# Kernel tuning notes

Measured on AMD Instinct MI355X. Metric: run time of the kernel, lower is better.

## Reference

```python
import jax, jax.numpy as jnp
import numpy as np

TRUST_W, SIM_W, STALE_W = 0.4, 0.4, 0.2
EPS = 1e-8  # torch cosine_similarity norm clamp


def setup_inputs() -> dict:
    key = jax.random.key(0)
    ks = jax.random.split(key, 6)
    B, D, E, C = 8192, 1024, 32, 256
    x = jax.random.normal(ks[0], (B, D), dtype=jnp.float32)
    expert_features = jax.random.normal(ks[1], (E, D), dtype=jnp.float32)
    trust = jax.random.uniform(ks[2], (E,), dtype=jnp.float32)
    staleness = jax.random.uniform(ks[3], (E,), dtype=jnp.float32)
    W = jax.random.normal(ks[4], (E, C, D), dtype=jnp.float32) * 0.02
    b = jax.random.normal(ks[5], (E, C), dtype=jnp.float32) * 0.02
    return {"x": x, "expert_features": expert_features, "trust": trust,
            "staleness": staleness, "W": W, "b": b, "k": 4}


def reference(x, expert_features, trust, staleness, W, b, k):
    # --- scoring: trust + cosine similarity + staleness, per (token, expert) ---
    xn = x / jnp.maximum(jnp.linalg.norm(x, axis=-1, keepdims=True), EPS)
    efn = expert_features / jnp.maximum(
        jnp.linalg.norm(expert_features, axis=-1, keepdims=True), EPS)
    cos = xn @ efn.T                              # [B, E]
    sim = (cos + 1.0) * 0.5
    stale_score = jnp.maximum(0.0, 1.0 - staleness)  # [E]
    scores = TRUST_W * trust + SIM_W * sim + STALE_W * stale_score  # [B, E]

    # --- top-k expert selection per token ---
    _, idx = jax.lax.top_k(scores, k)             # [B, k] int32

    # --- grouped expert heads: dense all-expert GEMM, then gather top-k ---
    all_out = jnp.einsum('bd,ecd->bec', x, W) + b  # [B, E, C]
    sel = jnp.take_along_axis(all_out, idx[:, :, None], axis=1)  # [B, k, C]
    return sel.mean(axis=1)                        # [B, C]
```

## Files before the change

### kernel.cpp

```cpp
#include <hip/hip_runtime.h>
#include <math.h>

#define KMAX 8
#define CSTRIDE 64

typedef short s16x8 __attribute__((ext_vector_type(8)));
typedef float f32x4 __attribute__((ext_vector_type(4)));

__device__ inline ushort f2bf(float f) {
    union { float f; unsigned u; } v; v.f = f;
    unsigned r = v.u + 0x7fffu + ((v.u >> 16) & 1u);
    return (ushort)(r >> 16);
}
__device__ inline float bf2f(ushort b) {
    union { unsigned u; float f; } v; v.u = ((unsigned)b) << 16; return v.f;
}

__device__ inline void gload_lds16(const void* g, void* l) {
    __builtin_amdgcn_global_load_lds(
        (const __attribute__((address_space(1))) unsigned int*)g,
        (__attribute__((address_space(3))) unsigned int*)l, 16, 0, 0);
}

__global__ void k_efnorm(const float* __restrict__ ef, int D,
                         double* __restrict__ efn, int* __restrict__ counts) {
    int e = blockIdx.x;
    int lane = threadIdx.x;
    if (lane == 0) counts[e * CSTRIDE] = 0;
    double s = 0.0;
    for (int i = lane; i < D; i += 64) {
        double v = (double)ef[(size_t)e * D + i];
        s = fma(v, v, s);
    }
    #pragma unroll
    for (int off = 32; off > 0; off >>= 1) s += __shfl_xor(s, off);
    if (lane == 0) efn[e] = sqrt(s);
}

__global__ __launch_bounds__(256) void k_prep_w(
    const float* __restrict__ W, const int* __restrict__ counts,
    int perExpF4, ushort* __restrict__ wbf, int* __restrict__ offs) {
    int e = blockIdx.y;
    if (blockIdx.x == 0 && e == 0 && threadIdx.x == 0) {
        int s = 0;
        for (int e2 = 0; e2 < 32; ++e2) { offs[e2] = s; s += counts[e2 * CSTRIDE]; }
    }
    if (counts[e * CSTRIDE] == 0) return;
    size_t base = (size_t)e * perExpF4;
    #pragma unroll
    for (int j = 0; j < 4; ++j) {
        int idx = (blockIdx.x * 4 + j) * 256 + threadIdx.x;
        if (idx < perExpF4) {
            float4 v = *(const float4*)&W[(base + idx) * 4];
            ushort4 u;
            u.x = f2bf(v.x); u.y = f2bf(v.y); u.z = f2bf(v.z); u.w = f2bf(v.w);
            *(ushort4*)&wbf[(base + idx) * 4] = u;
        }
    }
}

__global__ __launch_bounds__(256) void k_scores3a(
    const float* __restrict__ x, const float* __restrict__ ef,
    int D, int B, ushort* __restrict__ xbf,
    double* __restrict__ pacc, double* __restrict__ paxx)
{
    __shared__ float xs[16 * 64];
    __shared__ float efs[32 * 64];

    int tid = threadIdx.x;
    int tp = tid >> 4, eg = tid & 15;
    int g = blockIdx.x >> 1, h = blockIdx.x & 1;
    int tb = g * 16;
    int kbase = h * (D >> 1);
    int nch = D >> 7;

    int rx = tid >> 4, qx = tid & 15;
    int re0 = tid >> 4, re1 = 16 + (tid >> 4);
    int qe = tid & 15;

    float4 vx  = *(const float4*)&x[(size_t)(tb + rx) * D + kbase + qx * 4];
    float4 ve0 = *(const float4*)&ef[(size_t)re0 * D + kbase + qe * 4];
    float4 ve1 = *(const float4*)&ef[(size_t)re1 * D + kbase + qe * 4];

    double acc0 = 0.0, acc1 = 0.0, axx = 0.0;

    for (int ch = 0; ch < nch; ++ch) {
        int k0 = kbase + ch * 64;
        *(float4*)&xs[rx * 64 + ((qx ^ rx) << 2)] = vx;
        {
            ushort4 u;
            u.x = f2bf(vx.x); u.y = f2bf(vx.y); u.z = f2bf(vx.z); u.w = f2bf(vx.w);
            *(ushort4*)&xbf[(size_t)(tb + rx) * D + k0 + qx * 4] = u;
        }
        *(float4*)&efs[re0 * 64 + ((qe ^ (re0 & 15)) << 2)] = ve0;
        *(float4*)&efs[re1 * 64 + ((qe ^ (re1 & 15)) << 2)] = ve1;
        __syncthreads();

        if (ch + 1 < nch) {
            int k1 = kbase + (ch + 1) * 64;
            vx  = *(const float4*)&x[(size_t)(tb + rx) * D + k1 + qx * 4];
            ve0 = *(const float4*)&ef[(size_t)re0 * D + k1 + qe * 4];
            ve1 = *(const float4*)&ef[(size_t)re1 * D + k1 + qe * 4];
        }

        float a0 = 0.f, a1 = 0.f, ax = 0.f;
        #pragma unroll
        for (int q = 0; q < 16; ++q) {
            float4 xv = *(const float4*)&xs[tp * 64 + ((q ^ tp) << 2)];
            float4 e0 = *(const float4*)&efs[eg * 64 + ((q ^ eg) << 2)];
            float4 e1 = *(const float4*)&efs[(eg + 16) * 64 + ((q ^ eg) << 2)];
            a0 = fmaf(xv.x, e0.x, a0); a0 = fmaf(xv.y, e0.y, a0);
            a0 = fmaf(xv.z, e0.z, a0); a0 = fmaf(xv.w, e0.w, a0);
            a1 = fmaf(xv.x, e1.x, a1); a1 = fmaf(xv.y, e1.y, a1);
            a1 = fmaf(xv.z, e1.z, a1); a1 = fmaf(xv.w, e1.w, a1);
            ax = fmaf(xv.x, xv.x, ax); ax = fmaf(xv.y, xv.y, ax);
            ax = fmaf(xv.z, xv.z, ax); ax = fmaf(xv.w, xv.w, ax);
        }
        __syncthreads();
        acc0 += (double)a0; acc1 += (double)a1; axx += (double)ax;
    }

    int tt = tb + tp;
    pacc[(size_t)(h * 32 + eg) * B + tt] = acc0;
    pacc[(size_t)(h * 32 + eg + 16) * B + tt] = acc1;
    if (eg == 0) paxx[(size_t)h * B + tt] = axx;
}

__global__ __launch_bounds__(256) void k_scores3b(
    const float* __restrict__ trust, const float* __restrict__ stale,
    const double* __restrict__ efn, const double* __restrict__ pacc,
    const double* __restrict__ paxx, const int* __restrict__ kp,
    int B, int* __restrict__ counts, int* __restrict__ lists,
    int* __restrict__ sel)
{
    __shared__ double sc[128 * 33];
    __shared__ int bcnt[32];
    __shared__ int bbase[32];
    __shared__ unsigned char selb[128 * KMAX];
    __shared__ unsigned char lposb[128 * KMAX];

    int tid = threadIdx.x;
    int tk = tid & 127, eh = tid >> 7;
    int t = blockIdx.x * 128 + tk;

    if (tid < 32) bcnt[tid] = 0;

    double axx = paxx[t] + paxx[(size_t)B + t];
    double xn = fmax(sqrt(axx), 1e-8);
    #pragma unroll
    for (int j = 0; j < 16; ++j) {
        int e = eh * 16 + j;
        double dot = pacc[(size_t)e * B + t] + pacc[(size_t)(32 + e) * B + t];
        double en = fmax(efn[e], 1e-8);
        sc[tk * 33 + e] = 0.4 * (double)trust[e]
            + 0.2 * (dot / (xn * en) + 1.0)
            + 0.2 * fmax(0.0, 1.0 - (double)stale[e]);
    }
    __syncthreads();

    int kk = kp[0]; kk = kk < 1 ? 1 : (kk > KMAX ? KMAX : kk);

    if (tid < 128) {
        unsigned mask = 0;
        for (int p = 0; p < kk; ++p) {
            double bv = -1e300; int be = 0;
            #pragma unroll
            for (int e = 0; e < 32; ++e) {
                double v = sc[tid * 33 + e];
                if (!((mask >> e) & 1u) && v > bv) { bv = v; be = e; }
            }
            mask |= 1u << be;
            selb[tid * KMAX + p] = (unsigned char)be;
            lposb[tid * KMAX + p] = (unsigned char)atomicAdd(&bcnt[be], 1);
        }
    }
    __syncthreads();
    if (tid < 32) {
        int c = bcnt[tid];
        bbase[tid] = c ? atomicAdd(&counts[tid * CSTRIDE], c) : 0;
    }
    __syncthreads();
    if (tid < 128) {
        int tt = blockIdx.x * 128 + tid;
        for (int p = 0; p < kk; ++p) {
            int e = selb[tid * KMAX + p];
            int pos = bbase[e] + lposb[tid * KMAX + p];
            lists[(size_t)e * B + pos] = tt;
            sel[(size_t)tt * KMAX + p] = (e << 24) | pos;
        }
    }
}

__global__ __launch_bounds__(512) void k_moe3(
    const ushort* __restrict__ xbf, const ushort* __restrict__ wbf,
    const float* __restrict__ bias, const int* __restrict__ lists,
    const int* __restrict__ counts, const int* __restrict__ offs,
    const int* __restrict__ kp, int B, int C, int D,
    int usePart, ushort* __restrict__ part, float* __restrict__ out)
{
    int e = blockIdx.z;
    int cnt = counts[e * CSTRIDE];
    int row0 = blockIdx.x * 128;
    if (row0 >= cnt) return;
    int col0 = blockIdx.y * 128;
    int nt = min(128, cnt - row0);

    __shared__ ushort xs[128 * 64];
    __shared__ ushort wsh[128 * 64];
    __shared__ int toks[128];

    int tid = threadIdx.x;
    if (tid < 128) toks[tid] = (tid < nt) ? lists[(size_t)e * B + row0 + tid] : 0;
    __syncthreads();

    int lane = tid & 63, wid = tid >> 6;
    int wr = wid >> 1, wc = wid & 1;
    int l15 = lane & 15, l16 = lane >> 4;

    f32x4 acc[2][4];
    #pragma unroll
    for (int m = 0; m < 2; ++m)
        #pragma unroll
        for (int n = 0; n < 4; ++n) acc[m][n] = (f32x4){0.f, 0.f, 0.f, 0.f};

    int nch = D / 64;
    for (int ch = 0; ch < nch; ++ch) {
        int k0 = ch * 64;
        #pragma unroll
        for (int t = 0; t < 2; ++t) {
            int id = t * 512 + tid;
            int r = id >> 3, seg = id & 7;
            int ssw = (seg ^ (r & 7)) << 3;
            gload_lds16(&xbf[(size_t)toks[r] * D + k0 + ssw],
                        (char*)xs + (size_t)(t * 512 + wid * 64) * 16);
        }
        #pragma unroll
        for (int t = 0; t < 2; ++t) {
            int id = t * 512 + tid;
            int r = id >> 3, seg = id & 7;
            int ssw = (seg ^ (r & 7)) << 3;
            gload_lds16(&wbf[((size_t)e * C + col0 + r) * D + k0 + ssw],
                        (char*)wsh + (size_t)(t * 512 + wid * 64) * 16);
        }
        __syncthreads();
        #pragma unroll
        for (int ks = 0; ks < 2; ++ks) {
            s16x8 a[2], bfr[4];
            int sbase = ks * 4 + l16;
            #pragma unroll
            for (int m = 0; m < 2; ++m) {
                int r = wr * 32 + m * 16 + l15;
                a[m] = *(const s16x8*)&xs[r * 64 + ((sbase ^ (l15 & 7)) << 3)];
            }
            #pragma unroll
            for (int n = 0; n < 4; ++n) {
                int r = wc * 64 + n * 16 + l15;
                bfr[n] = *(const s16x8*)&wsh[r * 64 + ((sbase ^ (l15 & 7)) << 3)];
            }
            #pragma unroll
            for (int m = 0; m < 2; ++m)
                #pragma unroll
                for (int n = 0; n < 4; ++n)
                    acc[m][n] = __builtin_amdgcn_mfma_f32_16x16x32_bf16(
                        a[m], bfr[n], acc[m][n], 0, 0, 0);
        }
        __syncthreads();
    }

    int kk = kp[0]; kk = kk < 1 ? 1 : (kk > KMAX ? KMAX : kk);
    if (usePart) {
        int slotBase = offs[e] + row0;
        #pragma unroll
        for (int m = 0; m < 2; ++m) {
            int rbase = wr * 32 + m * 16 + l16 * 4;
            #pragma unroll
            for (int n = 0; n < 4; ++n) {
                int col = col0 + wc * 64 + n * 16 + l15;
                float bv = bias[(size_t)e * C + col];
                #pragma unroll
                for (int r = 0; r < 4; ++r) {
                    int rl = rbase + r;
                    if (rl < nt)
                        part[(size_t)(slotBase + rl) * C + col] =
                            f2bf(acc[m][n][r] + bv);
                }
            }
        }
    } else {
        float invk = 1.0f / (float)kk;
        #pragma unroll
        for (int m = 0; m < 2; ++m) {
            int rbase = wr * 32 + m * 16 + l16 * 4;
            #pragma unroll
            for (int n = 0; n < 4; ++n) {
                int col = col0 + wc * 64 + n * 16 + l15;
                float bv = bias[(size_t)e * C + col];
                #pragma unroll
                for (int r = 0; r < 4; ++r) {
                    int rl = rbase + r;
                    if (rl < nt)
                        atomicAdd(&out[(size_t)toks[rl] * C + col],
                                  invk * (acc[m][n][r] + bv));
                }
            }
        }
    }
}

__global__ __launch_bounds__(256) void k_combine(
    const ushort* __restrict__ part, const int* __restrict__ sel,
    const int* __restrict__ offs, const int* __restrict__ kp,
    int C, float* __restrict__ out)
{
    int kk = kp[0]; kk = kk < 1 ? 1 : (kk > KMAX ? KMAX : kk);
    float invk = 1.0f / (float)kk;
    int sub = threadIdx.x >> 6, lane = threadIdx.x & 63;
    int t = blockIdx.x * 4 + sub;
    for (int c = lane * 4; c < C; c += 256) {
        float s0 = 0.f, s1 = 0.f, s2 = 0.f, s3 = 0.f;
        for (int p = 0; p < kk; ++p) {
            int sv = sel[(size_t)t * KMAX + p];
            int slot = offs[sv >> 24] + (sv & 0xFFFFFF);
            ushort4 u = *(const ushort4*)&part[(size_t)slot * C + c];
            s0 += bf2f(u.x); s1 += bf2f(u.y); s2 += bf2f(u.z); s3 += bf2f(u.w);
        }
        float4 o = make_float4(invk * s0, invk * s1, invk * s2, invk * s3);
        *(float4*)&out[(size_t)t * C + c] = o;
    }
}

__global__ __launch_bounds__(256) void k_scores_legacy(
    const float* __restrict__ x, const float* __restrict__ ef,
    const float* __restrict__ trust, const float* __restrict__ stale,
    const double* __restrict__ efn, const int* __restrict__ kp,
    int D, int B, int* __restrict__ counts, int* __restrict__ lists)
{
    __shared__ float xs[32][72];
    __shared__ float efs[32][72];
    __shared__ double sc[32][33];

    int tid = threadIdx.x;
    int tl = tid >> 3, eg = tid & 7;
    int tb = blockIdx.x * 32;

    double acc[4] = {0, 0, 0, 0};
    double axx = 0.0;
    int nch = D / 64;

    for (int ch = 0; ch < nch; ++ch) {
        #pragma unroll
        for (int t = 0; t < 2; ++t) {
            int id = t * 256 + tid;
            int r = id >> 4, q = id & 15;
            float4 v = *(const float4*)&x[(size_t)(tb + r) * D + ch * 64 + q * 4];
            *(float4*)&xs[r][q * 4] = v;
            float4 w = *(const float4*)&ef[(size_t)r * D + ch * 64 + q * 4];
            *(float4*)&efs[r][q * 4] = w;
        }
        __syncthreads();
        #pragma unroll 4
        for (int q = 0; q < 16; ++q) {
            float4 xv = *(const float4*)&xs[tl][q * 4];
            double x0 = xv.x, x1 = xv.y, x2 = xv.z, x3 = xv.w;
            axx = fma(x0, x0, fma(x1, x1, fma(x2, x2, fma(x3, x3, axx))));
            #pragma unroll
            for (int j = 0; j < 4; ++j) {
                float4 ev = *(const float4*)&efs[eg + 8 * j][q * 4];
                acc[j] = fma(x0, (double)ev.x, acc[j]);
                acc[j] = fma(x1, (double)ev.y, acc[j]);
                acc[j] = fma(x2, (double)ev.z, acc[j]);
                acc[j] = fma(x3, (double)ev.w, acc[j]);
            }
        }
        __syncthreads();
    }

    double xn = fmax(sqrt(axx), 1e-8);
    #pragma unroll
    for (int j = 0; j < 4; ++j) {
        int e = eg + 8 * j;
        double en = fmax(efn[e], 1e-8);
        double cosv = acc[j] / (xn * en);
        sc[tl][e] = 0.4 * (double)trust[e] + 0.2 * (cosv + 1.0)
                  + 0.2 * fmax(0.0, 1.0 - (double)stale[e]);
    }
    __syncthreads();

    if (tid < 32) {
        int kk = kp[0]; kk = kk < 1 ? 1 : (kk > KMAX ? KMAX : kk);
        unsigned mask = 0;
        int t = tb + tid;
        for (int p = 0; p < kk; ++p) {
            double bv = -1e300; int be = 0;
            #pragma unroll
            for (int e = 0; e < 32; ++e) {
                double v = sc[tid][e];
                if (!((mask >> e) & 1u) && v > bv) { bv = v; be = e; }
            }
            mask |= 1u << be;
            int pos = atomicAdd(&counts[be * CSTRIDE], 1);
            lists[(size_t)be * B + pos] = t;
        }
    }
}

__global__ __launch_bounds__(512) void k_moe_f32(
    const float* __restrict__ x, const float* __restrict__ W,
    const float* __restrict__ bias, const int* __restrict__ lists,
    const int* __restrict__ counts, const int* __restrict__ kp,
    int B, int C, int D, float* __restrict__ out)
{
    int e = blockIdx.z;
    int cnt = counts[e * CSTRIDE];
    int row0 = blockIdx.x * 128;
    if (row0 >= cnt) return;
    int col0 = blockIdx.y * 256;
    int nt = min(128, cnt - row0);

    __shared__ ushort xs[128 * 72];
    __shared__ ushort wsh[256 * 72];
    __shared__ int toks[128];

    int tid = threadIdx.x;
    if (tid < 128) toks[tid] = (tid < nt) ? lists[(size_t)e * B + row0 + tid] : 0;
    __syncthreads();

    int lane = tid & 63, wid = tid >> 6;
    int wr = wid >> 2, wc = wid & 3;
    int l15 = lane & 15, l16 = lane >> 4;

    f32x4 acc[4][4];
    #pragma unroll
    for (int m = 0; m < 4; ++m)
        #pragma unroll
        for (int n = 0; n < 4; ++n) acc[m][n] = (f32x4){0.f, 0.f, 0.f, 0.f};

    int nch = D / 64;
    for (int ch = 0; ch < nch; ++ch) {
        int k0 = ch * 64;
        #pragma unroll
        for (int t = 0; t < 4; ++t) {
            int id = t * 512 + tid;
            int r = id >> 4, q = id & 15;
            float4 v = (r < nt)
                ? *(const float4*)&x[(size_t)toks[r] * D + k0 + q * 4]
                : make_float4(0.f, 0.f, 0.f, 0.f);
            ushort4 u;
            u.x = f2bf(v.x); u.y = f2bf(v.y); u.z = f2bf(v.z); u.w = f2bf(v.w);
            *(ushort4*)&xs[r * 72 + q * 4] = u;
        }
        #pragma unroll
        for (int t = 0; t < 8; ++t) {
            int id = t * 512 + tid;
            int r = id >> 4, q = id & 15;
            float4 v = *(const float4*)&W[((size_t)e * C + col0 + r) * D + k0 + q * 4];
            ushort4 u;
            u.x = f2bf(v.x); u.y = f2bf(v.y); u.z = f2bf(v.z); u.w = f2bf(v.w);
            *(ushort4*)&wsh[r * 72 + q * 4] = u;
        }
        __syncthreads();
        #pragma unroll
        for (int ks = 0; ks < 2; ++ks) {
            s16x8 a[4], bfr[4];
            #pragma unroll
            for (int m = 0; m < 4; ++m)
                a[m] = *(const s16x8*)&xs[(wr * 64 + m * 16 + l15) * 72 + ks * 32 + l16 * 8];
            #pragma unroll
            for (int n = 0; n < 4; ++n)
                bfr[n] = *(const s16x8*)&wsh[(wc * 64 + n * 16 + l15) * 72 + ks * 32 + l16 * 8];
            #pragma unroll
            for (int m = 0; m < 4; ++m)
                #pragma unroll
                for (int n = 0; n < 4; ++n)
                    acc[m][n] = __builtin_amdgcn_mfma_f32_16x16x32_bf16(
                        a[m], bfr[n], acc[m][n], 0, 0, 0);
        }
        __syncthreads();
    }

    int kk = kp[0]; kk = kk < 1 ? 1 : (kk > KMAX ? KMAX : kk);
    float invk = 1.0f / (float)kk;
    #pragma unroll
    for (int m = 0; m < 4; ++m) {
        int rbase = wr * 64 + m * 16 + l16 * 4;
        #pragma unroll
        for (int n = 0; n < 4; ++n) {
            int col = col0 + wc * 64 + n * 16 + l15;
            float bv = bias[(size_t)e * C + col];
            #pragma unroll
            for (int r = 0; r < 4; ++r) {
                int rl = rbase + r;
                if (rl < nt)
                    atomicAdd(&out[(size_t)toks[rl] * C + col],
                              invk * (acc[m][n][r] + bv));
            }
        }
    }
}

extern "C" void kernel_launch(void* const* d_in, const int* in_sizes, int n_in,
                              void* d_out, int out_size, void* d_ws, size_t ws_size,
                              hipStream_t stream) {
    const float* x     = (const float*)d_in[0];
    const float* ef    = (const float*)d_in[1];
    const float* trust = (const float*)d_in[2];
    const float* stale = (const float*)d_in[3];
    const float* W     = (const float*)d_in[4];
    const float* b     = (const float*)d_in[5];
    const int*   kp    = (const int*)d_in[6];

    int E = in_sizes[2];
    int D = in_sizes[1] / E;
    int B = in_sizes[0] / D;
    int C = in_sizes[5] / E;
    float* out = (float*)d_out;

    char* ws = (char*)d_ws;
    double* efn   = (double*)ws;
    int*    counts= (int*)(ws + 256);
    size_t off_offs = 256 + 32 * CSTRIDE * 4;
    int*    offs  = (int*)(ws + off_offs);
    size_t off_sel = off_offs + 256;
    int*    sel   = (int*)(ws + off_sel);
    size_t off_lists = off_sel + (size_t)B * KMAX * 4;
    int*    lists = (int*)(ws + off_lists);
    size_t off_pacc = off_lists + (size_t)E * B * 4;
    off_pacc = (off_pacc + 255) & ~(size_t)255;
    double* pacc  = (double*)(ws + off_pacc);
    size_t off_paxx = off_pacc + (size_t)64 * B * 8;
    double* paxx  = (double*)(ws + off_paxx);
    size_t off_xbf = off_paxx + (size_t)2 * B * 8;
    off_xbf = (off_xbf + 255) & ~(size_t)255;
    ushort* xbf = (ushort*)(ws + off_xbf);
    size_t off_wbf = off_xbf + (size_t)B * D * 2;
    ushort* wbf = (ushort*)(ws + off_wbf);
    size_t off_part = off_wbf + (size_t)E * C * D * 2;
    off_part = (off_part + 255) & ~(size_t)255;
    ushort* part = (ushort*)(ws + off_part);
    size_t need_mid  = off_part;
    size_t need_full = off_part + (size_t)B * KMAX * C * 2;

    bool fullPath = ws_size >= need_mid;
    int usePart = (fullPath && ws_size >= need_full) ? 1 : 0;

    if (!usePart)
        hipMemsetAsync(d_out, 0, (size_t)out_size * sizeof(float), stream);

    k_efnorm<<<E, 64, 0, stream>>>(ef, D, efn, counts);

    if (fullPath) {
        k_scores3a<<<(B / 16) * 2, 256, 0, stream>>>(x, ef, D, B, xbf,
                                                     pacc, paxx);
        k_scores3b<<<B / 128, 256, 0, stream>>>(trust, stale, efn, pacc, paxx,
                                                kp, B, counts, lists, sel);
        int perExpF4 = (C * D) / 4;
        dim3 wgrid((perExpF4 + 1023) / 1024, E);
        k_prep_w<<<wgrid, 256, 0, stream>>>(W, counts, perExpF4, wbf, offs);
        dim3 grid((B + 127) / 128, C / 128, E);
        k_moe3<<<grid, 512, 0, stream>>>(xbf, wbf, b, lists, counts, offs, kp,
                                         B, C, D, usePart, part, out);
        if (usePart)
            k_combine<<<B / 4, 256, 0, stream>>>(part, sel, offs, kp, C, out);
    } else {
        k_scores_legacy<<<B / 32, 256, 0, stream>>>(x, ef, trust, stale, efn,
                                                    kp, D, B, counts, lists);
        dim3 grid((B + 127) / 128, C / 256, E);
        k_moe_f32<<<grid, 512, 0, stream>>>(x, W, b, lists, counts, kp,
                                            B, C, D, out);
    }
}
```

Measured before the change: 81.97 us.

## Split scoring K-dimension four ways and fold expert-norm kernel into scoring launch

The partial dot-product scoring kernel now splits the D reduction into four quarters instead of two, doubling the block count so more of the GPU is occupied, with the combine step summing four partials. The separate expert-feature norm kernel is merged into the same launch as extra tail blocks that also zero the counts, removing one kernel launch. The cost is more partial-sum memory traffic (pacc grows to 128*B doubles) and a larger workspace.

```diff
diff --git a/kernel.cpp b/kernel.cpp
--- a/kernel.cpp
+++ b/kernel.cpp
@@ -61,18 +61,37 @@
 
 __global__ __launch_bounds__(256) void k_scores3a(
     const float* __restrict__ x, const float* __restrict__ ef,
-    int D, int B, ushort* __restrict__ xbf,
-    double* __restrict__ pacc, double* __restrict__ paxx)
+    int D, int B, int nSB4, ushort* __restrict__ xbf,
+    double* __restrict__ pacc, double* __restrict__ paxx,
+    double* __restrict__ efn, int* __restrict__ counts)
 {
     __shared__ float xs[16 * 64];
     __shared__ float efs[32 * 64];
+    __shared__ double wsum[4];
 
     int tid = threadIdx.x;
+
+    if ((int)blockIdx.x >= nSB4) {
+        int e = blockIdx.x - nSB4;
+        if (tid == 0) counts[e * CSTRIDE] = 0;
+        double s = 0.0;
+        for (int i = tid; i < D; i += 256) {
+            double v = (double)ef[(size_t)e * D + i];
+            s = fma(v, v, s);
+        }
+        #pragma unroll
+        for (int off = 32; off > 0; off >>= 1) s += __shfl_xor(s, off);
+        if ((tid & 63) == 0) wsum[tid >> 6] = s;
+        __syncthreads();
+        if (tid == 0) efn[e] = sqrt(wsum[0] + wsum[1] + wsum[2] + wsum[3]);
+        return;
+    }
+
     int tp = tid >> 4, eg = tid & 15;
-    int g = blockIdx.x >> 1, h = blockIdx.x & 1;
+    int g = blockIdx.x >> 2, h = blockIdx.x & 3;
     int tb = g * 16;
-    int kbase = h * (D >> 1);
-    int nch = D >> 7;
+    int kbase = h * (D >> 2);
+    int nch = D >> 8;
 
     int rx = tid >> 4, qx = tid & 15;
     int re0 = tid >> 4, re1 = 16 + (tid >> 4);
@@ -145,12 +164,14 @@
 
     if (tid < 32) bcnt[tid] = 0;
 
-    double axx = paxx[t] + paxx[(size_t)B + t];
+    double axx = (paxx[t] + paxx[(size_t)B + t])
+               + (paxx[(size_t)2 * B + t] + paxx[(size_t)3 * B + t]);
     double xn = fmax(sqrt(axx), 1e-8);
     #pragma unroll
     for (int j = 0; j < 16; ++j) {
         int e = eh * 16 + j;
-        double dot = pacc[(size_t)e * B + t] + pacc[(size_t)(32 + e) * B + t];
+        double dot = (pacc[(size_t)e * B + t] + pacc[(size_t)(32 + e) * B + t])
+                   + (pacc[(size_t)(64 + e) * B + t] + pacc[(size_t)(96 + e) * B + t]);
         double en = fmax(efn[e], 1e-8);
         sc[tk * 33 + e] = 0.4 * (double)trust[e]
             + 0.2 * (dot / (xn * en) + 1.0)
@@ -527,9 +548,9 @@
     size_t off_pacc = off_lists + (size_t)E * B * 4;
     off_pacc = (off_pacc + 255) & ~(size_t)255;
     double* pacc  = (double*)(ws + off_pacc);
-    size_t off_paxx = off_pacc + (size_t)64 * B * 8;
+    size_t off_paxx = off_pacc + (size_t)128 * B * 8;
     double* paxx  = (double*)(ws + off_paxx);
-    size_t off_xbf = off_paxx + (size_t)2 * B * 8;
+    size_t off_xbf = off_paxx + (size_t)4 * B * 8;
     off_xbf = (off_xbf + 255) & ~(size_t)255;
     ushort* xbf = (ushort*)(ws + off_xbf);
     size_t off_wbf = off_xbf + (size_t)B * D * 2;
@@ -546,11 +567,10 @@
     if (!usePart)
         hipMemsetAsync(d_out, 0, (size_t)out_size * sizeof(float), stream);
 
-    k_efnorm<<<E, 64, 0, stream>>>(ef, D, efn, counts);
-
     if (fullPath) {
-        k_scores3a<<<(B / 16) * 2, 256, 0, stream>>>(x, ef, D, B, xbf,
-                                                     pacc, paxx);
+        int nSB4 = (B / 16) * 4;
+        k_scores3a<<<nSB4 + E, 256, 0, stream>>>(x, ef, D, B, nSB4, xbf,
+                                                 pacc, paxx, efn, counts);
         k_scores3b<<<B / 128, 256, 0, stream>>>(trust, stale, efn, pacc, paxx,
                                                 kp, B, counts, lists, sel);
         int perExpF4 = (C * D) / 4;
@@ -562,6 +582,7 @@
         if (usePart)
             k_combine<<<B / 4, 256, 0, stream>>>(part, sel, offs, kp, C, out);
     } else {
+        k_efnorm<<<E, 64, 0, stream>>>(ef, D, efn, counts);
         k_scores_legacy<<<B / 32, 256, 0, stream>>>(x, ef, trust, stale, efn,
                                                     kp, D, B, counts, lists);
         dim3 grid((B + 127) / 128, C / 256, E);
```

Result: faster. 78.38 us, median of 2 (-4.4%).
